# Kernel tuning notes

Measured on AMD Instinct MI355X. Metric: run time of the kernel, lower is better.

Reference implementation:

```python
import jax, jax.numpy as jnp
import numpy as np

NUM_HEADS = 12
EPS = 1e-4


def setup_inputs() -> dict:
    key = jax.random.key(0)
    k1, k2, k3 = jax.random.split(key, 3)
    C = 768
    B, N = 128, 196  # B = b * num_frames = 8 * 16
    x = jax.random.normal(k1, (B, N, C), dtype=jnp.float32)
    W_qkv = jax.random.normal(k2, (3 * C, C), dtype=jnp.float32) * 0.02
    W_proj = jax.random.normal(k3, (C, C), dtype=jnp.float32) * 0.02
    b_proj = jnp.zeros((C,), dtype=jnp.float32)
    return {"x": x, "W_qkv": W_qkv, "W_proj": W_proj, "b_proj": b_proj,
            "num_frames": 16}


def reference(x, W_qkv, W_proj, b_proj, num_frames):
    B, N, C = x.shape
    h = NUM_HEADS
    e = C // h
    # qkv projection (no bias), split k-first then heads: 'b n (k h e)'
    qkv = (x @ W_qkv.T).reshape(B, N, 3, h, e)
    q, k, v = qkv[:, :, 0], qkv[:, :, 1], qkv[:, :, 2]  # [B, N, h, e]
    q_ = jax.nn.relu(q)
    k_ = jax.nn.relu(k)
    # fold frames into the sequence: (b f) n -> b (f n)
    b = B // num_frames
    S = num_frames * N
    q_ = q_.reshape(b, S, h, e)
    k_ = k_.reshape(b, S, h, e)
    v_ = v.reshape(b, S, h, e)
    # kv trick: kv[b,h,e,d] = sum_s k[b,s,h,e] v[b,s,h,d]
    kv = jnp.einsum('bshe,bshd->bhed', k_, v_)
    k_sum = k_.sum(axis=1)  # [b, h, e]
    z = 1.0 / (jnp.einsum('bshe,bhe->bsh', q_, k_sum) + EPS)  # [b, S, h]
    out = jnp.einsum('bshe,bhed->bshd', q_, kv) * z[..., None]  # [b, S, h, e]
    out = out.reshape(B, N, C)
    # output projection (dropouts are identity at eval)
    return out @ W_proj.T + b_proj
```

## Files before the change

### kernel.cpp

```cpp
#include <hip/hip_runtime.h>
#include <hip/hip_bf16.h>

#define EPS_Z 1e-4f

typedef __attribute__((ext_vector_type(8))) short bf16x8;
typedef __attribute__((ext_vector_type(4))) float f32x4;

__device__ __forceinline__ float b2f(short s) {
    union { unsigned u; float f; } cv;
    cv.u = ((unsigned)(unsigned short)s) << 16;
    return cv.f;
}

__device__ __forceinline__ void gld_lds16(const __hip_bfloat16* g, __hip_bfloat16* l) {
    __builtin_amdgcn_global_load_lds(
        (__attribute__((address_space(1))) void*)(g),
        (__attribute__((address_space(3))) void*)(l),
        16, 0, 0);
}

__global__ __launch_bounds__(256)
void cvt_all(const float* __restrict__ x, const float* __restrict__ wq,
             const float* __restrict__ wp,
             __hip_bfloat16* __restrict__ xb, __hip_bfloat16* __restrict__ wqb,
             __hip_bfloat16* __restrict__ wpb)
{
    const int N4X = 25088 * 768 / 4;
    const int N4Q = 2304 * 768 / 4;
    const int N4P = 768 * 768 / 4;
    int i = blockIdx.x * 256 + threadIdx.x;
    const float* src;
    __hip_bfloat16* dst;
    int idx;
    if (i < N4X)            { src = x;  dst = xb;  idx = i; }
    else if (i < N4X + N4Q) { src = wq; dst = wqb; idx = i - N4X; }
    else if (i < N4X + N4Q + N4P) { src = wp; dst = wpb; idx = i - N4X - N4Q; }
    else return;
    float4 v = ((const float4*)src)[idx];
    union { short4 s; __hip_bfloat16 h[4]; } o;
    o.h[0] = __float2bfloat16(v.x);
    o.h[1] = __float2bfloat16(v.y);
    o.h[2] = __float2bfloat16(v.z);
    o.h[3] = __float2bfloat16(v.w);
    ((short4*)dst)[idx] = o.s;
}

template<int MODE, typename CT>
__global__ __launch_bounds__(256, 3)
void gemm_bt(const __hip_bfloat16* __restrict__ A,
             const __hip_bfloat16* __restrict__ B,
             CT* __restrict__ C,
             const float* __restrict__ bias,
             int K, int N, int gx)
{
    __shared__ __align__(16) __hip_bfloat16 As[128 * 64];
    __shared__ __align__(16) __hip_bfloat16 Bs[128 * 64];
    const int g = blockIdx.x;
    const int gp = (g & 7) * ((int)gridDim.x >> 3) + (g >> 3);
    const int bx = gp % gx;
    const int by = gp / gx;

    const int tid = threadIdx.x;
    const int w = tid >> 6;
    const int l = tid & 63;
    const int wr = (w >> 1) * 64;
    const int wc = (w & 1) * 64;
    const int l15 = l & 15;
    const int lq = l >> 4;
    const int rx = l15 & 7;

    f32x4 acc[4][4] = {};

    const int srow8 = l >> 3;
    const int scol = (((l & 7) ^ (l >> 3)) << 3);

    const __hip_bfloat16* Ab = A + (size_t)by * 128 * K;
    const __hip_bfloat16* Bb = B + (size_t)bx * 128 * K;

    for (int k0 = 0; k0 < K; k0 += 64) {
        __syncthreads();
        #pragma unroll
        for (int i = 0; i < 4; ++i) {
            const int chunk = w * 4 + i;
            const int row = chunk * 8 + srow8;
            gld_lds16(Ab + (size_t)row * K + (k0 + scol), As + chunk * 512);
            gld_lds16(Bb + (size_t)row * K + (k0 + scol), Bs + chunk * 512);
        }
        __syncthreads();
        #pragma unroll
        for (int kk = 0; kk < 64; kk += 32) {
            const int kb = (kk >> 3) + lq;
            const int col = (kb ^ rx) << 3;
            bf16x8 a[4], b[4];
            #pragma unroll
            for (int i = 0; i < 4; ++i)
                a[i] = *(const bf16x8*)(As + (wr + i * 16 + l15) * 64 + col);
            #pragma unroll
            for (int j = 0; j < 4; ++j)
                b[j] = *(const bf16x8*)(Bs + (wc + j * 16 + l15) * 64 + col);
            #pragma unroll
            for (int i = 0; i < 4; ++i)
                #pragma unroll
                for (int j = 0; j < 4; ++j)
                    acc[i][j] = __builtin_amdgcn_mfma_f32_16x16x32_bf16(a[i], b[j], acc[i][j], 0, 0, 0);
        }
    }

    const int crow0 = by * 128 + wr + lq * 4;
    const int ccol0 = bx * 128 + wc + l15;
    #pragma unroll
    for (int i = 0; i < 4; ++i) {
        #pragma unroll
        for (int j = 0; j < 4; ++j) {
            const int gc = ccol0 + j * 16;
            const float badd = (MODE == 2) ? bias[gc] : 0.0f;
            #pragma unroll
            for (int r = 0; r < 4; ++r) {
                const int gr = crow0 + i * 16 + r;
                float v = acc[i][j][r];
                if (MODE == 1 && gc < 1536) v = fmaxf(v, 0.0f);
                if (MODE == 2) v += badd;
                if (MODE == 1)
                    ((__hip_bfloat16*)C)[(size_t)gr * N + gc] = __float2bfloat16(v);
                else
                    ((float*)C)[(size_t)gr * N + gc] = v;
            }
        }
    }
}

__global__ __launch_bounds__(256)
void kv_mfma_kernel(const __hip_bfloat16* __restrict__ qkv,
                    float* __restrict__ kvp, float* __restrict__ ksump)
{
    const int SPLIT = 7;
    const int bh = blockIdx.x / SPLIT;
    const int ck = blockIdx.x % SPLIT;
    const int b = bh / 12, h = bh % 12;

    __shared__ __align__(16) __hip_bfloat16 kT[64 * 40];
    __shared__ __align__(16) __hip_bfloat16 vT[64 * 40];

    const int tid = threadIdx.x;
    const int w = tid >> 6, l = tid & 63;
    const int l15 = l & 15, lq = l >> 4;

    const int half = tid >> 7;
    const int idx  = tid & 127;
    const int e0 = (idx >> 4) * 8;
    const int sp = idx & 15;

    const size_t rowbase = (size_t)b * 3136 * 2304 + (half ? 1536 : 768) + h * 64 + e0;
    __hip_bfloat16* Tdst = half ? vT : kT;

    f32x4 acc[4] = {};
    f32x4 accks = {};

    bf16x8 ones;
    #pragma unroll
    for (int i = 0; i < 8; ++i) ones[i] = (short)0x3F80;

    const int s_begin = ck * 448;
    const int s_end = s_begin + 448;

    bf16x8 r0 = *(const bf16x8*)(qkv + rowbase + (size_t)(s_begin + 2 * sp) * 2304);
    bf16x8 r1 = *(const bf16x8*)(qkv + rowbase + (size_t)(s_begin + 2 * sp + 1) * 2304);

    for (int s0 = s_begin; s0 < s_end; s0 += 32) {
        __syncthreads();
        #pragma unroll
        for (int qq = 0; qq < 8; ++qq) {
            unsigned pk = ((unsigned)(unsigned short)r0[qq]) |
                          (((unsigned)(unsigned short)r1[qq]) << 16);
            *(unsigned*)(Tdst + (e0 + qq) * 40 + 2 * sp) = pk;
        }
        __syncthreads();
        if (s0 + 32 < s_end) {
            r0 = *(const bf16x8*)(qkv + rowbase + (size_t)(s0 + 32 + 2 * sp) * 2304);
            r1 = *(const bf16x8*)(qkv + rowbase + (size_t)(s0 + 33 + 2 * sp) * 2304);
        }
        bf16x8 a = *(const bf16x8*)(vT + (w * 16 + l15) * 40 + lq * 8);
        bf16x8 bfr[4];
        #pragma unroll
        for (int j = 0; j < 4; ++j)
            bfr[j] = *(const bf16x8*)(kT + (j * 16 + l15) * 40 + lq * 8);
        #pragma unroll
        for (int j = 0; j < 4; ++j)
            acc[j] = __builtin_amdgcn_mfma_f32_16x16x32_bf16(a, bfr[j], acc[j], 0, 0, 0);
        accks = __builtin_amdgcn_mfma_f32_16x16x32_bf16(ones, bfr[w], accks, 0, 0, 0);
    }

    float* kvdst = kvp + ((size_t)(bh * SPLIT + ck) << 12);
    #pragma unroll
    for (int j = 0; j < 4; ++j) {
        const int col = j * 16 + l15;
        #pragma unroll
        for (int r = 0; r < 4; ++r) {
            const int row = w * 16 + lq * 4 + r;
            kvdst[row * 64 + col] = acc[j][r];
        }
    }
    if (lq == 0)
        ksump[(size_t)(bh * SPLIT + ck) * 64 + w * 16 + l15] = accks[0];
}

__global__ __launch_bounds__(256)
void kv_reduce(const float* __restrict__ kvp, const float* __restrict__ ksump,
               __hip_bfloat16* __restrict__ kvb, float* __restrict__ ksum)
{
    const int SPLIT = 7;
    const int bh = blockIdx.x;
    const int tid = threadIdx.x;

    const float* base = kvp + ((size_t)bh * SPLIT << 12) + tid * 16;
    float4 s0 = {}, s1 = {}, s2 = {}, s3 = {};
    #pragma unroll
    for (int p = 0; p < SPLIT; ++p) {
        const float* bp = base + ((size_t)p << 12);
        float4 a0 = *(const float4*)(bp + 0);
        float4 a1 = *(const float4*)(bp + 4);
        float4 a2 = *(const float4*)(bp + 8);
        float4 a3 = *(const float4*)(bp + 12);
        s0.x += a0.x; s0.y += a0.y; s0.z += a0.z; s0.w += a0.w;
        s1.x += a1.x; s1.y += a1.y; s1.z += a1.z; s1.w += a1.w;
        s2.x += a2.x; s2.y += a2.y; s2.z += a2.z; s2.w += a2.w;
        s3.x += a3.x; s3.y += a3.y; s3.z += a3.z; s3.w += a3.w;
    }
    union { bf16x8 v; __hip_bfloat16 h[8]; } o0, o1;
    o0.h[0] = __float2bfloat16(s0.x); o0.h[1] = __float2bfloat16(s0.y);
    o0.h[2] = __float2bfloat16(s0.z); o0.h[3] = __float2bfloat16(s0.w);
    o0.h[4] = __float2bfloat16(s1.x); o0.h[5] = __float2bfloat16(s1.y);
    o0.h[6] = __float2bfloat16(s1.z); o0.h[7] = __float2bfloat16(s1.w);
    o1.h[0] = __float2bfloat16(s2.x); o1.h[1] = __float2bfloat16(s2.y);
    o1.h[2] = __float2bfloat16(s2.z); o1.h[3] = __float2bfloat16(s2.w);
    o1.h[4] = __float2bfloat16(s3.x); o1.h[5] = __float2bfloat16(s3.y);
    o1.h[6] = __float2bfloat16(s3.z); o1.h[7] = __float2bfloat16(s3.w);
    __hip_bfloat16* dst = kvb + ((size_t)bh << 12) + tid * 16;
    *(bf16x8*)(dst + 0) = o0.v;
    *(bf16x8*)(dst + 8) = o1.v;

    if (tid < 64) {
        float t = 0.0f;
        #pragma unroll
        for (int p = 0; p < SPLIT; ++p)
            t += ksump[(size_t)(bh * SPLIT + p) * 64 + tid];
        ksum[(size_t)bh * 64 + tid] = t;
    }
}

__global__ __launch_bounds__(256)
void attn_mfma2(const __hip_bfloat16* __restrict__ qkv,
                const __hip_bfloat16* __restrict__ kvb,
                const float* __restrict__ ksumg,
                __hip_bfloat16* __restrict__ att)
{
    const int bh = blockIdx.x / 25;
    const int u  = blockIdx.x % 25;
    const int b = bh / 12, h = bh % 12;
    const int tid = threadIdx.x;
    const int w = tid >> 6, l = tid & 63;
    const int l15 = l & 15, lq = l >> 4;

    const __hip_bfloat16* kvh = kvb + ((size_t)bh << 12);
    bf16x8 b0[4], b1[4];
    #pragma unroll
    for (int j = 0; j < 4; ++j) {
        b0[j] = *(const bf16x8*)(kvh + (j * 16 + l15) * 64 + lq * 8);
        b1[j] = *(const bf16x8*)(kvh + (j * 16 + l15) * 64 + 32 + lq * 8);
    }
    const float* ks = ksumg + (bh << 6);
    float kse[8], kse1[8];
    *(float4*)(kse)      = *(const float4*)(ks + lq * 8);
    *(float4*)(kse + 4)  = *(const float4*)(ks + lq * 8 + 4);
    *(float4*)(kse1)     = *(const float4*)(ks + 32 + lq * 8);
    *(float4*)(kse1 + 4) = *(const float4*)(ks + 32 + lq * 8 + 4);

    #pragma unroll
    for (int t = 0; t < 2; ++t) {
        const int mt = u * 2 + t;
        if (mt >= 49) break;
        const size_t m0 = (size_t)b * 3136 + (size_t)mt * 64 + w * 16;

        const __hip_bfloat16* qrow = qkv + (m0 + l15) * 2304 + h * 64;
        bf16x8 aq0 = *(const bf16x8*)(qrow + lq * 8);
        bf16x8 aq1 = *(const bf16x8*)(qrow + 32 + lq * 8);

        float zp = 0.0f;
        #pragma unroll
        for (int j = 0; j < 8; ++j)
            zp += b2f(aq0[j]) * kse[j] + b2f(aq1[j]) * kse1[j];
        zp += __shfl_xor(zp, 16);
        zp += __shfl_xor(zp, 32);
        const float zr = 1.0f / (zp + EPS_Z);

        f32x4 acc[4] = {};
        #pragma unroll
        for (int j = 0; j < 4; ++j) {
            acc[j] = __builtin_amdgcn_mfma_f32_16x16x32_bf16(aq0, b0[j], acc[j], 0, 0, 0);
            acc[j] = __builtin_amdgcn_mfma_f32_16x16x32_bf16(aq1, b1[j], acc[j], 0, 0, 0);
        }

        float zrow[4];
        #pragma unroll
        for (int r = 0; r < 4; ++r) zrow[r] = __shfl(zr, lq * 4 + r);

        #pragma unroll
        for (int j = 0; j < 4; ++j) {
            const int col = j * 16 + l15;
            #pragma unroll
            for (int r = 0; r < 4; ++r) {
                const int row = lq * 4 + r;
                att[(m0 + row) * 768 + h * 64 + col] = __float2bfloat16(acc[j][r] * zrow[r]);
            }
        }
    }
}

extern "C" void kernel_launch(void* const* d_in, const int* in_sizes, int n_in,
                              void* d_out, int out_size, void* d_ws, size_t ws_size,
                              hipStream_t stream)
{
    const float* x      = (const float*)d_in[0];
    const float* W_qkv  = (const float*)d_in[1];
    const float* W_proj = (const float*)d_in[2];
    const float* b_proj = (const float*)d_in[3];
    float* out = (float*)d_out;

    const int M = 25088, K = 768, N1 = 2304, N2 = 768;
    const int SPLIT = 7;

    __hip_bfloat16* qkv = (__hip_bfloat16*)d_ws;
    __hip_bfloat16* xb  = qkv + (size_t)M * N1;
    __hip_bfloat16* wqb = xb + (size_t)M * K;
    __hip_bfloat16* wpb = wqb + (size_t)N1 * K;
    float* kvp   = (float*)(wpb + (size_t)N2 * K);
    float* ksump = kvp + (size_t)SPLIT * 96 * 4096;
    float* ksum  = ksump + (size_t)SPLIT * 96 * 64;
    __hip_bfloat16* kvb = (__hip_bfloat16*)(ksum + 96 * 64);
    __hip_bfloat16* att = xb;

    const int CVT_TOT = (M * K + N1 * K + N2 * K) / 4;
    cvt_all<<<(CVT_TOT + 255) / 256, 256, 0, stream>>>(x, W_qkv, W_proj, xb, wqb, wpb);

    gemm_bt<1, __hip_bfloat16><<<(M / 128) * (N1 / 128), 256, 0, stream>>>(
        xb, wqb, qkv, nullptr, K, N1, N1 / 128);
    kv_mfma_kernel<<<96 * SPLIT, 256, 0, stream>>>(qkv, kvp, ksump);
    kv_reduce<<<96, 256, 0, stream>>>(kvp, ksump, kvb, ksum);
    attn_mfma2<<<96 * 25, 256, 0, stream>>>(qkv, kvb, ksum, att);
    gemm_bt<2, float><<<(M / 128) * (N2 / 128), 256, 0, stream>>>(
        att, wpb, out, b_proj, K, N2, N2 / 128);
}
```

Baseline: 336.2 us.

## Split QKV GEMM in halves, fix XCD remap, restructure attention over heads per block

The QKV projection GEMM is launched as two half-M launches. The XCD block remapping is rewritten so it handles grids not divisible by 8, and the GEMM occupancy hint rises from 3 to 4 blocks. The attention kernel becomes 128-thread blocks, each owning 32 rows and looping over all 12 heads, in place of one head per block. The aim is better L2/XCD locality and tail balance. The costs are an extra launch and more serial per-block work in attention.

```diff
diff --git a/kernel.cpp b/kernel.cpp
--- a/kernel.cpp
+++ b/kernel.cpp
@@ -46,7 +46,7 @@
 }
 
 template<int MODE, typename CT>
-__global__ __launch_bounds__(256, 3)
+__global__ __launch_bounds__(256, 4)
 void gemm_bt(const __hip_bfloat16* __restrict__ A,
              const __hip_bfloat16* __restrict__ B,
              CT* __restrict__ C,
@@ -55,8 +55,11 @@
 {
     __shared__ __align__(16) __hip_bfloat16 As[128 * 64];
     __shared__ __align__(16) __hip_bfloat16 Bs[128 * 64];
+    const int nwg = (int)gridDim.x;
     const int g = blockIdx.x;
-    const int gp = (g & 7) * ((int)gridDim.x >> 3) + (g >> 3);
+    const int xcd = g & 7, lin = g >> 3;
+    const int q = nwg >> 3, r = nwg & 7;
+    const int gp = (xcd < r ? xcd * (q + 1) : r * (q + 1) + (xcd - r) * q) + lin;
     const int bx = gp % gx;
     const int by = gp / gx;
 
@@ -115,9 +118,9 @@
             const int gc = ccol0 + j * 16;
             const float badd = (MODE == 2) ? bias[gc] : 0.0f;
             #pragma unroll
-            for (int r = 0; r < 4; ++r) {
-                const int gr = crow0 + i * 16 + r;
-                float v = acc[i][j][r];
+            for (int r2 = 0; r2 < 4; ++r2) {
+                const int gr = crow0 + i * 16 + r2;
+                float v = acc[i][j][r2];
                 if (MODE == 1 && gc < 1536) v = fmaxf(v, 0.0f);
                 if (MODE == 2) v += badd;
                 if (MODE == 1)
@@ -248,38 +251,39 @@
     }
 }
 
-__global__ __launch_bounds__(256)
-void attn_mfma2(const __hip_bfloat16* __restrict__ qkv,
+__global__ __launch_bounds__(128)
+void attn_mfma3(const __hip_bfloat16* __restrict__ qkv,
                 const __hip_bfloat16* __restrict__ kvb,
                 const float* __restrict__ ksumg,
                 __hip_bfloat16* __restrict__ att)
 {
-    const int bh = blockIdx.x / 25;
-    const int u  = blockIdx.x % 25;
-    const int b = bh / 12, h = bh % 12;
+    const int x = blockIdx.x;
+    const int b = x / 98;
+    const int rem = x % 98;
+    const int mt = rem >> 1, half = rem & 1;
     const int tid = threadIdx.x;
     const int w = tid >> 6, l = tid & 63;
     const int l15 = l & 15, lq = l >> 4;
 
-    const __hip_bfloat16* kvh = kvb + ((size_t)bh << 12);
-    bf16x8 b0[4], b1[4];
-    #pragma unroll
-    for (int j = 0; j < 4; ++j) {
-        b0[j] = *(const bf16x8*)(kvh + (j * 16 + l15) * 64 + lq * 8);
-        b1[j] = *(const bf16x8*)(kvh + (j * 16 + l15) * 64 + 32 + lq * 8);
-    }
-    const float* ks = ksumg + (bh << 6);
-    float kse[8], kse1[8];
-    *(float4*)(kse)      = *(const float4*)(ks + lq * 8);
-    *(float4*)(kse + 4)  = *(const float4*)(ks + lq * 8 + 4);
-    *(float4*)(kse1)     = *(const float4*)(ks + 32 + lq * 8);
-    *(float4*)(kse1 + 4) = *(const float4*)(ks + 32 + lq * 8 + 4);
-
-    #pragma unroll
-    for (int t = 0; t < 2; ++t) {
-        const int mt = u * 2 + t;
-        if (mt >= 49) break;
-        const size_t m0 = (size_t)b * 3136 + (size_t)mt * 64 + w * 16;
+    const size_t m0 = (size_t)b * 3136 + (size_t)mt * 64 + half * 32 + w * 16;
+
+    #pragma unroll 1
+    for (int h = 0; h < 12; ++h) {
+        const int bh = b * 12 + h;
+
+        const __hip_bfloat16* kvh = kvb + ((size_t)bh << 12);
+        bf16x8 b0[4], b1[4];
+        #pragma unroll
+        for (int j = 0; j < 4; ++j) {
+            b0[j] = *(const bf16x8*)(kvh + (j * 16 + l15) * 64 + lq * 8);
+            b1[j] = *(const bf16x8*)(kvh + (j * 16 + l15) * 64 + 32 + lq * 8);
+        }
+        const float* ks = ksumg + (bh << 6);
+        float kse[8], kse1[8];
+        *(float4*)(kse)      = *(const float4*)(ks + lq * 8);
+        *(float4*)(kse + 4)  = *(const float4*)(ks + lq * 8 + 4);
+        *(float4*)(kse1)     = *(const float4*)(ks + 32 + lq * 8);
+        *(float4*)(kse1 + 4) = *(const float4*)(ks + 32 + lq * 8 + 4);
 
         const __hip_bfloat16* qrow = qkv + (m0 + l15) * 2304 + h * 64;
         bf16x8 aq0 = *(const bf16x8*)(qrow + lq * 8);
@@ -328,6 +332,7 @@
 
     const int M = 25088, K = 768, N1 = 2304, N2 = 768;
     const int SPLIT = 7;
+    const int MH = M / 2;
 
     __hip_bfloat16* qkv = (__hip_bfloat16*)d_ws;
     __hip_bfloat16* xb  = qkv + (size_t)M * N1;
@@ -342,11 +347,14 @@
     const int CVT_TOT = (M * K + N1 * K + N2 * K) / 4;
     cvt_all<<<(CVT_TOT + 255) / 256, 256, 0, stream>>>(x, W_qkv, W_proj, xb, wqb, wpb);
 
-    gemm_bt<1, __hip_bfloat16><<<(M / 128) * (N1 / 128), 256, 0, stream>>>(
+    gemm_bt<1, __hip_bfloat16><<<(MH / 128) * (N1 / 128), 256, 0, stream>>>(
         xb, wqb, qkv, nullptr, K, N1, N1 / 128);
+    gemm_bt<1, __hip_bfloat16><<<(MH / 128) * (N1 / 128), 256, 0, stream>>>(
+        xb + (size_t)MH * K, wqb, qkv + (size_t)MH * N1, nullptr, K, N1, N1 / 128);
+
     kv_mfma_kernel<<<96 * SPLIT, 256, 0, stream>>>(qkv, kvp, ksump);
     kv_reduce<<<96, 256, 0, stream>>>(kvp, ksump, kvb, ksum);
-    attn_mfma2<<<96 * 25, 256, 0, stream>>>(qkv, kvb, ksum, att);
+    attn_mfma3<<<784, 128, 0, stream>>>(qkv, kvb, ksum, att);
     gemm_bt<2, float><<<(M / 128) * (N2 / 128), 256, 0, stream>>>(
         att, wpb, out, b_proj, K, N2, N2 / 128);
 }
```

Result: slower. 360.4 us (+7.2%).
